# Optimization experiments

Hardware: AMD Instinct MI355X
Metric: run time of the kernel (lower is better)

The kernel has to match this reference:

```python
import jax, jax.numpy as jnp
import numpy as np

EPS = 1e-8  # matches torch F.cosine_similarity eps


def setup_inputs() -> dict:
    key = jax.random.key(0)
    k1, k2, k3 = jax.random.split(key, 3)
    S, B, H = 16, 512, 2048
    OGLogits = jax.random.normal(k1, (B, H), dtype=jnp.float32)
    enhancedSamplesLogits = jax.random.normal(k2, (S, B, H), dtype=jnp.float32)
    W = jax.random.normal(k3, (H, H), dtype=jnp.float32) * (1.0 / np.sqrt(H))
    b = jnp.zeros((H,), dtype=jnp.float32)
    return {"OGLogits": OGLogits, "enhancedSamplesLogits": enhancedSamplesLogits, "W": W, "b": b}


def reference(OGLogits, enhancedSamplesLogits, W, b):
    # Original torch code builds the full (S*B, B) cosine-similarity matrix and
    # keeps only the diagonal via an eye mask; mathematically that equals the
    # per-pair cosine similarity cos(enhanced[s,b], OG[b]), computed directly here.
    e_norm = jnp.linalg.norm(enhancedSamplesLogits, axis=-1)          # (S, B)
    o_norm = jnp.linalg.norm(OGLogits, axis=-1)                       # (B,)
    dots = jnp.einsum('sbh,bh->sb', enhancedSamplesLogits, OGLogits)  # (S, B)
    sims = dots / jnp.maximum(e_norm * o_norm[None, :], EPS)          # (S, B)
    weighted = enhancedSamplesLogits * sims[..., None]                # (S, B, H)
    weightedRep = weighted.mean(axis=0)                               # (B, H)
    return weightedRep @ W.T + b                                      # (B, H)
```

## Files before the change

kernel.cpp:

```cpp
#include <hip/hip_runtime.h>

#define S_DIM 16
#define B_DIM 512
#define H_DIM 2048
#define EPS 1e-8f

typedef short bf16x8 __attribute__((ext_vector_type(8)));
typedef float f32x16 __attribute__((ext_vector_type(16)));

__device__ __forceinline__ unsigned short f2bf(float f) {
    union { float f; unsigned int u; } v; v.f = f;
    unsigned int u = v.u;
    unsigned int r = (u + 0x7fffu + ((u >> 16) & 1u)) >> 16;
    return (unsigned short)r;
}

__device__ __forceinline__ float dot4(const float4& a, const float4& b) {
    return a.x*b.x + a.y*b.y + a.z*b.z + a.w*b.w;
}

__global__ __launch_bounds__(512) void fused_kernel(
    const float* __restrict__ OG, const float* __restrict__ E,
    const float* __restrict__ W, unsigned short* __restrict__ wrep,
    unsigned short* __restrict__ Wb) {
    const int b = blockIdx.x;
    const int t = threadIdx.x;
    const int lane = t & 63;
    const int wave = t >> 6;

    __shared__ float4 buf[8][512];

    const float4* e4a = (const float4*)(E + ((size_t)wave * B_DIM + b) * H_DIM);
    const float4* e4b = (const float4*)(E + ((size_t)(wave + 8) * B_DIM + b) * H_DIM);
    const float4* og4 = (const float4*)(OG + (size_t)b * H_DIM);

    float4 ea[8], eb[8], og[8];
    #pragma unroll
    for (int i = 0; i < 8; ++i) {
        const int c = (i + wave) & 7;
        ea[i] = e4a[c * 64 + lane];
        eb[i] = e4b[c * 64 + lane];
        og[i] = og4[c * 64 + lane];
    }

    float da = 0.f, na = 0.f, db = 0.f, nb = 0.f, o2 = 0.f;
    #pragma unroll
    for (int i = 0; i < 8; ++i) {
        da += dot4(ea[i], og[i]);
        na += dot4(ea[i], ea[i]);
        db += dot4(eb[i], og[i]);
        nb += dot4(eb[i], eb[i]);
        o2 += dot4(og[i], og[i]);
    }
    #pragma unroll
    for (int m = 32; m >= 1; m >>= 1) {
        da += __shfl_xor(da, m, 64);
        na += __shfl_xor(na, m, 64);
        db += __shfl_xor(db, m, 64);
        nb += __shfl_xor(nb, m, 64);
        o2 += __shfl_xor(o2, m, 64);
    }
    const float onorm = sqrtf(o2);
    const float sima = da / fmaxf(sqrtf(na) * onorm, EPS);
    const float simb = db / fmaxf(sqrtf(nb) * onorm, EPS);

    #pragma unroll
    for (int i = 0; i < 8; ++i) {
        const int c = (i + wave) & 7;
        float4 v;
        v.x = ea[i].x * sima + eb[i].x * simb;
        v.y = ea[i].y * sima + eb[i].y * simb;
        v.z = ea[i].z * sima + eb[i].z * simb;
        v.w = ea[i].w * sima + eb[i].w * simb;
        buf[wave][c * 64 + lane] = v;
    }
    __syncthreads();

    float4 s = buf[0][t];
    #pragma unroll
    for (int w = 1; w < 8; ++w) {
        float4 v = buf[w][t];
        s.x += v.x; s.y += v.y; s.z += v.z; s.w += v.w;
    }
    const float sc = 1.f / (float)S_DIM;
    ushort4 ob;
    ob.x = f2bf(s.x * sc); ob.y = f2bf(s.y * sc);
    ob.z = f2bf(s.z * sc); ob.w = f2bf(s.w * sc);
    ((ushort4*)wrep)[(size_t)b * (H_DIM / 4) + t] = ob;

    const float4* w4 = (const float4*)W;
    #pragma unroll
    for (int j = 0; j < 4; ++j) {
        const size_t idx = (size_t)b * 2048 + j * 512 + t;
        float4 v = w4[idx];
        ushort4 c;
        c.x = f2bf(v.x); c.y = f2bf(v.y); c.z = f2bf(v.z); c.w = f2bf(v.w);
        ((ushort4*)Wb)[idx] = c;
    }
}

__global__ __launch_bounds__(256) void gemm_kernel(
    const unsigned short* __restrict__ A, const unsigned short* __restrict__ Wb,
    const float* __restrict__ bias, float* __restrict__ out) {
    const int n0 = blockIdx.x * 64;
    const int m0 = blockIdx.y * 64;

    __shared__ unsigned short As[2][64][72];
    __shared__ unsigned short Bs[2][64][72];

    const int t = threadIdx.x;
    const int lane = t & 63;
    const int wave = t >> 6;
    const int wm = (wave & 1) * 32;
    const int wn = (wave >> 1) * 32;

    const int lr = t >> 2, lq = t & 3;
    const unsigned short* ap = A  + (size_t)(m0 + lr) * H_DIM + lq * 16;
    const unsigned short* bp = Wb + (size_t)(n0 + lr) * H_DIM + lq * 16;

    f32x16 acc0 = {0.f,0.f,0.f,0.f,0.f,0.f,0.f,0.f,
                   0.f,0.f,0.f,0.f,0.f,0.f,0.f,0.f};
    f32x16 acc1 = {0.f,0.f,0.f,0.f,0.f,0.f,0.f,0.f,
                   0.f,0.f,0.f,0.f,0.f,0.f,0.f,0.f};

    const int row = lane & 31;
    const int hi = lane >> 5;

    uint4 a0 = *(const uint4*)(ap);
    uint4 a1 = *(const uint4*)(ap + 8);
    uint4 b0 = *(const uint4*)(bp);
    uint4 b1 = *(const uint4*)(bp + 8);
    *(uint4*)&As[0][lr][lq * 16]     = a0;
    *(uint4*)&As[0][lr][lq * 16 + 8] = a1;
    *(uint4*)&Bs[0][lr][lq * 16]     = b0;
    *(uint4*)&Bs[0][lr][lq * 16 + 8] = b1;
    __syncthreads();

    for (int ki = 0; ki < 32; ++ki) {
        const int cur = ki & 1, nxt = cur ^ 1;
        if (ki + 1 < 32) {
            a0 = *(const uint4*)(ap + (ki + 1) * 64);
            a1 = *(const uint4*)(ap + (ki + 1) * 64 + 8);
            b0 = *(const uint4*)(bp + (ki + 1) * 64);
            b1 = *(const uint4*)(bp + (ki + 1) * 64 + 8);
        }
        #pragma unroll
        for (int ks = 0; ks < 2; ++ks) {
            bf16x8 afA = *(const bf16x8*)&As[cur][wm + row][ks * 16 + hi * 8];
            bf16x8 bfA = *(const bf16x8*)&Bs[cur][wn + row][ks * 16 + hi * 8];
            acc0 = __builtin_amdgcn_mfma_f32_32x32x16_bf16(afA, bfA, acc0, 0, 0, 0);
            bf16x8 afB = *(const bf16x8*)&As[cur][wm + row][(ks + 2) * 16 + hi * 8];
            bf16x8 bfB = *(const bf16x8*)&Bs[cur][wn + row][(ks + 2) * 16 + hi * 8];
            acc1 = __builtin_amdgcn_mfma_f32_32x32x16_bf16(afB, bfB, acc1, 0, 0, 0);
        }
        if (ki + 1 < 32) {
            *(uint4*)&As[nxt][lr][lq * 16]     = a0;
            *(uint4*)&As[nxt][lr][lq * 16 + 8] = a1;
            *(uint4*)&Bs[nxt][lr][lq * 16]     = b0;
            *(uint4*)&Bs[nxt][lr][lq * 16 + 8] = b1;
        }
        __syncthreads();
    }

    const int col = lane & 31;
    const float bias0 = bias[n0 + wn + col];
    #pragma unroll
    for (int r = 0; r < 16; ++r) {
        const int mr = (r & 3) + 8 * (r >> 2) + 4 * hi;
        out[(size_t)(m0 + wm + mr) * H_DIM + n0 + wn + col] = acc0[r] + acc1[r] + bias0;
    }
}

extern "C" void kernel_launch(void* const* d_in, const int* in_sizes, int n_in,
                              void* d_out, int out_size, void* d_ws, size_t ws_size,
                              hipStream_t stream) {
    const float* OG   = (const float*)d_in[0];
    const float* E    = (const float*)d_in[1];
    const float* W    = (const float*)d_in[2];
    const float* bias = (const float*)d_in[3];
    float* out = (float*)d_out;

    unsigned short* wrep = (unsigned short*)d_ws;
    unsigned short* Wb   = wrep + (size_t)B_DIM * H_DIM;

    fused_kernel<<<B_DIM, 512, 0, stream>>>(OG, E, W, wrep, Wb);
    gemm_kernel<<<dim3(H_DIM / 64, B_DIM / 64), 256, 0, stream>>>(wrep, Wb, bias, out);
}
```

Before: 126.1 us.

## Overlap W conversion with reductions, share OG via LDS, swizzle and deepen GEMM prefetch

In the fused kernel, the W-to-bf16 conversion loads are issued early and their stores are interleaved with the cosine-similarity work. OG is now loaded once per block into shared memory instead of once per wave, and its norm comes from a block-level reduction. The GEMM gets an XOR-swizzled LDS layout to cut bank conflicts, a two-stage register prefetch that keeps two K-tiles in flight, and a 1D grid that maps neighbouring blocks along M so they share W tiles. The extra register pressure and barriers are traded for better latency hiding.

```diff
diff --git a/kernel.cpp b/kernel.cpp
--- a/kernel.cpp
+++ b/kernel.cpp
@@ -19,7 +19,7 @@
     return a.x*b.x + a.y*b.y + a.z*b.z + a.w*b.w;
 }
 
-__global__ __launch_bounds__(512) void fused_kernel(
+__global__ __launch_bounds__(512, 4) void fused_kernel(
     const float* __restrict__ OG, const float* __restrict__ E,
     const float* __restrict__ W, unsigned short* __restrict__ wrep,
     unsigned short* __restrict__ Wb) {
@@ -29,28 +29,55 @@
     const int wave = t >> 6;
 
     __shared__ float4 buf[8][512];
+    __shared__ float4 ogs[512];
+    __shared__ float red[8];
+
+    const float4* w4 = (const float4*)W;
+    ushort4* wb4 = (ushort4*)Wb;
+    const size_t wbase = (size_t)b * 2048 + t;
+
+    float4 wv0 = w4[wbase];
+    float4 wv1 = w4[wbase + 512];
+    const float4* og4 = (const float4*)(OG + (size_t)b * H_DIM);
+    float4 o = og4[t];
 
     const float4* e4a = (const float4*)(E + ((size_t)wave * B_DIM + b) * H_DIM);
     const float4* e4b = (const float4*)(E + ((size_t)(wave + 8) * B_DIM + b) * H_DIM);
-    const float4* og4 = (const float4*)(OG + (size_t)b * H_DIM);
-
-    float4 ea[8], eb[8], og[8];
+    float4 ea[8], eb[8];
     #pragma unroll
     for (int i = 0; i < 8; ++i) {
-        const int c = (i + wave) & 7;
-        ea[i] = e4a[c * 64 + lane];
-        eb[i] = e4b[c * 64 + lane];
-        og[i] = og4[c * 64 + lane];
-    }
-
-    float da = 0.f, na = 0.f, db = 0.f, nb = 0.f, o2 = 0.f;
+        ea[i] = e4a[i * 64 + lane];
+        eb[i] = e4b[i * 64 + lane];
+    }
+    float4 wv2 = w4[wbase + 1024];
+    float4 wv3 = w4[wbase + 1536];
+
+    ogs[t] = o;
+    float p = dot4(o, o);
+    #pragma unroll
+    for (int m = 32; m >= 1; m >>= 1) p += __shfl_xor(p, m, 64);
+    if (lane == 0) red[wave] = p;
+
+    {
+        ushort4 c0, c1;
+        c0.x = f2bf(wv0.x); c0.y = f2bf(wv0.y); c0.z = f2bf(wv0.z); c0.w = f2bf(wv0.w);
+        c1.x = f2bf(wv1.x); c1.y = f2bf(wv1.y); c1.z = f2bf(wv1.z); c1.w = f2bf(wv1.w);
+        wb4[wbase] = c0;
+        wb4[wbase + 512] = c1;
+    }
+    __syncthreads();
+
+    float og2 = 0.f;
+    #pragma unroll
+    for (int w = 0; w < 8; ++w) og2 += red[w];
+    const float onorm = sqrtf(og2);
+
+    float da = 0.f, na = 0.f, db = 0.f, nb = 0.f;
     #pragma unroll
     for (int i = 0; i < 8; ++i) {
-        da += dot4(ea[i], og[i]);
-        na += dot4(ea[i], ea[i]);
-        db += dot4(eb[i], og[i]);
-        nb += dot4(eb[i], eb[i]);
-        o2 += dot4(og[i], og[i]);
+        float4 g = ogs[i * 64 + lane];
+        da += dot4(ea[i], g); na += dot4(ea[i], ea[i]);
+        db += dot4(eb[i], g); nb += dot4(eb[i], eb[i]);
     }
     #pragma unroll
     for (int m = 32; m >= 1; m >>= 1) {
@@ -58,21 +85,25 @@
         na += __shfl_xor(na, m, 64);
         db += __shfl_xor(db, m, 64);
         nb += __shfl_xor(nb, m, 64);
-        o2 += __shfl_xor(o2, m, 64);
-    }
-    const float onorm = sqrtf(o2);
+    }
     const float sima = da / fmaxf(sqrtf(na) * onorm, EPS);
     const float simb = db / fmaxf(sqrtf(nb) * onorm, EPS);
 
     #pragma unroll
     for (int i = 0; i < 8; ++i) {
-        const int c = (i + wave) & 7;
         float4 v;
         v.x = ea[i].x * sima + eb[i].x * simb;
         v.y = ea[i].y * sima + eb[i].y * simb;
         v.z = ea[i].z * sima + eb[i].z * simb;
         v.w = ea[i].w * sima + eb[i].w * simb;
-        buf[wave][c * 64 + lane] = v;
+        buf[wave][i * 64 + lane] = v;
+    }
+    {
+        ushort4 c2, c3;
+        c2.x = f2bf(wv2.x); c2.y = f2bf(wv2.y); c2.z = f2bf(wv2.z); c2.w = f2bf(wv2.w);
+        c3.x = f2bf(wv3.x); c3.y = f2bf(wv3.y); c3.z = f2bf(wv3.z); c3.w = f2bf(wv3.w);
+        wb4[wbase + 1024] = c2;
+        wb4[wbase + 1536] = c3;
     }
     __syncthreads();
 
@@ -87,26 +118,17 @@
     ob.x = f2bf(s.x * sc); ob.y = f2bf(s.y * sc);
     ob.z = f2bf(s.z * sc); ob.w = f2bf(s.w * sc);
     ((ushort4*)wrep)[(size_t)b * (H_DIM / 4) + t] = ob;
-
-    const float4* w4 = (const float4*)W;
-    #pragma unroll
-    for (int j = 0; j < 4; ++j) {
-        const size_t idx = (size_t)b * 2048 + j * 512 + t;
-        float4 v = w4[idx];
-        ushort4 c;
-        c.x = f2bf(v.x); c.y = f2bf(v.y); c.z = f2bf(v.z); c.w = f2bf(v.w);
-        ((ushort4*)Wb)[idx] = c;
-    }
 }
 
 __global__ __launch_bounds__(256) void gemm_kernel(
     const unsigned short* __restrict__ A, const unsigned short* __restrict__ Wb,
     const float* __restrict__ bias, float* __restrict__ out) {
-    const int n0 = blockIdx.x * 64;
-    const int m0 = blockIdx.y * 64;
-
-    __shared__ unsigned short As[2][64][72];
-    __shared__ unsigned short Bs[2][64][72];
+    const int bid = blockIdx.x;
+    const int m0 = (bid & 7) * 64;
+    const int n0 = (bid >> 3) * 64;
+
+    __shared__ unsigned short As[2][64 * 72];
+    __shared__ unsigned short Bs[2][64 * 72];
 
     const int t = threadIdx.x;
     const int lane = t & 63;
@@ -118,6 +140,10 @@
     const unsigned short* ap = A  + (size_t)(m0 + lr) * H_DIM + lq * 16;
     const unsigned short* bp = Wb + (size_t)(n0 + lr) * H_DIM + lq * 16;
 
+    const int sw = (lr & 7) << 4;
+    const int w0 = lr * 72 + (((lq * 32) ^ sw) >> 1);
+    const int w1 = lr * 72 + (((lq * 32 + 16) ^ sw) >> 1);
+
     f32x16 acc0 = {0.f,0.f,0.f,0.f,0.f,0.f,0.f,0.f,
                    0.f,0.f,0.f,0.f,0.f,0.f,0.f,0.f};
     f32x16 acc1 = {0.f,0.f,0.f,0.f,0.f,0.f,0.f,0.f,
@@ -125,42 +151,72 @@
 
     const int row = lane & 31;
     const int hi = lane >> 5;
-
-    uint4 a0 = *(const uint4*)(ap);
-    uint4 a1 = *(const uint4*)(ap + 8);
-    uint4 b0 = *(const uint4*)(bp);
-    uint4 b1 = *(const uint4*)(bp + 8);
-    *(uint4*)&As[0][lr][lq * 16]     = a0;
-    *(uint4*)&As[0][lr][lq * 16 + 8] = a1;
-    *(uint4*)&Bs[0][lr][lq * 16]     = b0;
-    *(uint4*)&Bs[0][lr][lq * 16 + 8] = b1;
+    const int rbase = (wm + row) * 72;
+    const int rsw = ((row & 7) << 4);
+    int roffA[4], roffB[4];
+    #pragma unroll
+    for (int ks = 0; ks < 4; ++ks) {
+        const int x = (ks * 32 + hi * 16) ^ rsw;
+        roffA[ks] = rbase + (x >> 1);
+        roffB[ks] = (wn + row) * 72 + (x >> 1);
+    }
+
+    uint4 ra0 = *(const uint4*)(ap);
+    uint4 ra1 = *(const uint4*)(ap + 8);
+    uint4 rb0 = *(const uint4*)(bp);
+    uint4 rb1 = *(const uint4*)(bp + 8);
+    uint4 sa0 = *(const uint4*)(ap + 64);
+    uint4 sa1 = *(const uint4*)(ap + 72);
+    uint4 sb0 = *(const uint4*)(bp + 64);
+    uint4 sb1 = *(const uint4*)(bp + 72);
+    *(uint4*)&As[0][w0] = ra0;
+    *(uint4*)&As[0][w1] = ra1;
+    *(uint4*)&Bs[0][w0] = rb0;
+    *(uint4*)&Bs[0][w1] = rb1;
     __syncthreads();
 
-    for (int ki = 0; ki < 32; ++ki) {
-        const int cur = ki & 1, nxt = cur ^ 1;
-        if (ki + 1 < 32) {
-            a0 = *(const uint4*)(ap + (ki + 1) * 64);
-            a1 = *(const uint4*)(ap + (ki + 1) * 64 + 8);
-            b0 = *(const uint4*)(bp + (ki + 1) * 64);
-            b1 = *(const uint4*)(bp + (ki + 1) * 64 + 8);
+    #define MFMA_TILE(BUF)                                                        \
+    {                                                                             \
+        _Pragma("unroll")                                                         \
+        for (int ks = 0; ks < 2; ++ks) {                                          \
+            bf16x8 afA = *(const bf16x8*)&As[BUF][roffA[ks]];                     \
+            bf16x8 bfA = *(const bf16x8*)&Bs[BUF][roffB[ks]];                     \
+            acc0 = __builtin_amdgcn_mfma_f32_32x32x16_bf16(afA, bfA, acc0, 0,0,0);\
+            bf16x8 afB = *(const bf16x8*)&As[BUF][roffA[ks + 2]];                 \
+            bf16x8 bfB = *(const bf16x8*)&Bs[BUF][roffB[ks + 2]];                 \
+            acc1 = __builtin_amdgcn_mfma_f32_32x32x16_bf16(afB, bfB, acc1, 0,0,0);\
+        }                                                                         \
+    }
+
+    for (int ki = 0; ki < 32; ki += 2) {
+        if (ki + 2 < 32) {
+            ra0 = *(const uint4*)(ap + (ki + 2) * 64);
+            ra1 = *(const uint4*)(ap + (ki + 2) * 64 + 8);
+            rb0 = *(const uint4*)(bp + (ki + 2) * 64);
+            rb1 = *(const uint4*)(bp + (ki + 2) * 64 + 8);
         }
-        #pragma unroll
-        for (int ks = 0; ks < 2; ++ks) {
-            bf16x8 afA = *(const bf16x8*)&As[cur][wm + row][ks * 16 + hi * 8];
-            bf16x8 bfA = *(const bf16x8*)&Bs[cur][wn + row][ks * 16 + hi * 8];
-            acc0 = __builtin_amdgcn_mfma_f32_32x32x16_bf16(afA, bfA, acc0, 0, 0, 0);
-            bf16x8 afB = *(const bf16x8*)&As[cur][wm + row][(ks + 2) * 16 + hi * 8];
-            bf16x8 bfB = *(const bf16x8*)&Bs[cur][wn + row][(ks + 2) * 16 + hi * 8];
-            acc1 = __builtin_amdgcn_mfma_f32_32x32x16_bf16(afB, bfB, acc1, 0, 0, 0);
+        MFMA_TILE(0);
+        *(uint4*)&As[1][w0] = sa0;
+        *(uint4*)&As[1][w1] = sa1;
+        *(uint4*)&Bs[1][w0] = sb0;
+        *(uint4*)&Bs[1][w1] = sb1;
+        __syncthreads();
+        if (ki + 3 < 32) {
+            sa0 = *(const uint4*)(ap + (ki + 3) * 64);
+            sa1 = *(const uint4*)(ap + (ki + 3) * 64 + 8);
+            sb0 = *(const uint4*)(bp + (ki + 3) * 64);
+            sb1 = *(const uint4*)(bp + (ki + 3) * 64 + 8);
         }
-        if (ki + 1 < 32) {
-            *(uint4*)&As[nxt][lr][lq * 16]     = a0;
-            *(uint4*)&As[nxt][lr][lq * 16 + 8] = a1;
-            *(uint4*)&Bs[nxt][lr][lq * 16]     = b0;
-            *(uint4*)&Bs[nxt][lr][lq * 16 + 8] = b1;
+        MFMA_TILE(1);
+        if (ki + 2 < 32) {
+            *(uint4*)&As[0][w0] = ra0;
+            *(uint4*)&As[0][w1] = ra1;
+            *(uint4*)&Bs[0][w0] = rb0;
+            *(uint4*)&Bs[0][w1] = rb1;
+            __syncthreads();
         }
-        __syncthreads();
-    }
+    }
+    #undef MFMA_TILE
 
     const int col = lane & 31;
     const float bias0 = bias[n0 + wn + col];
@@ -184,5 +240,5 @@
     unsigned short* Wb   = wrep + (size_t)B_DIM * H_DIM;
 
     fused_kernel<<<B_DIM, 512, 0, stream>>>(OG, E, W, wrep, Wb);
-    gemm_kernel<<<dim3(H_DIM / 64, B_DIM / 64), 256, 0, stream>>>(wrep, Wb, bias, out);
-}
+    gemm_kernel<<<256, 256, 0, stream>>>(wrep, Wb, bias, out);
+}
```

Measured after the change: 124.8 us. About the same (-1.1%).
